# Kernel optimization log

Measured on AMD Instinct MI355X. Metric: run time of the kernel, lower is better.

Reference implementation:

```python
import jax, jax.numpy as jnp
import numpy as np

EMBEDDING_DIM = 128


def _position_encoding_init(n_position, emb_dim):
    # positions 1..n_position, angle[pos, j] = pos / 10000^(2*(j//2)/emb_dim)
    pos = jnp.arange(1, n_position + 1, dtype=jnp.float32)[:, None]  # [S,1]
    j = jnp.arange(emb_dim, dtype=jnp.float32)[None, :]              # [1,D]
    angle = pos / jnp.power(10000.0, 2.0 * jnp.floor(j / 2.0) / emb_dim)  # [S,D]
    # faithful to the original: rows 1: get sin/cos, row 0 stays raw
    pe = angle
    pe = pe.at[1:, 0::2].set(jnp.sin(angle[1:, 0::2]))
    pe = pe.at[1:, 1::2].set(jnp.cos(angle[1:, 1::2]))
    return pe.astype(jnp.float32)


def setup_inputs() -> dict:
    key = jax.random.key(0)
    k1, k2, k3 = jax.random.split(key, 3)
    B, S = 128, 2048
    x = jax.random.normal(k1, (B, S, 2), dtype=jnp.float32)
    # solutions / best_solutions must be permutations of 0..S-1 per row
    solutions = jax.vmap(lambda k: jax.random.permutation(k, S))(jax.random.split(k2, B)).astype(jnp.int64)
    best_solutions = jax.vmap(lambda k: jax.random.permutation(k, S))(jax.random.split(k3, B)).astype(jnp.int64)
    return {"x": x, "solutions": solutions, "best_solutions": best_solutions}


def reference(x, solutions, best_solutions):
    B, S = solutions.shape
    pe = _position_encoding_init(S, EMBEDDING_DIM)  # [S, D]
    # visited_time[b, i] = position at which node i is visited = argsort of the tour
    visited_time = jnp.argsort(solutions, axis=1)            # [B, S]
    best_visited_time = jnp.argsort(best_solutions, axis=1)  # [B, S]
    pos_enc = pe[visited_time]            # [B, S, D] gather over the table
    best_pos_enc = pe[best_visited_time]  # [B, S, D]
    return pos_enc, best_pos_enc
```

## Files before the change

kernel.cpp:

```cpp
#include <hip/hip_runtime.h>
#include <math.h>

#define BB 128
#define SS 2048
#define DD 128
#define BS (BB * SS)
#define BLOCKS 8192
#define ROWSTRIDE (BLOCKS * 8)

typedef float f4 __attribute__((ext_vector_type(4)));

__global__ __launch_bounds__(256) void fused_scatter_kernel(
        const int* __restrict__ sol, const int* __restrict__ best,
        float* __restrict__ out) {
    const int t    = threadIdx.x;
    const int lane = t & 31;
    const int rib  = t >> 5;
    const int base = blockIdx.x * 8 + rib;
    const int i    = base & (SS - 1);

    const float c = -13.287712379549449f / 64.0f;
    const float invf0 = exp2f(c * (float)(2 * lane));
    const float invf1 = exp2f(c * (float)(2 * lane + 1));
    const float a0 = (float)(i + 1) * invf0;
    const float a1 = (float)(i + 1) * invf1;
    f4 v;
    if (i == 0) {
        v[0] = a0; v[1] = a0; v[2] = a1; v[3] = a1;
    } else {
        float s0, c0, s1, c1;
        sincosf(a0, &s0, &c0);
        sincosf(a1, &s1, &c1);
        v[0] = s0; v[1] = c0; v[2] = s1; v[3] = c1;
    }

    #pragma unroll
    for (int h = 0; h < 2; ++h) {
        const int* __restrict__ perm = h ? best : sol;
        float* __restrict__ outh = out + (size_t)h * BS * DD;
        #pragma unroll
        for (int it = 0; it < 4; ++it) {
            const int k    = base + it * ROWSTRIDE;
            const int node = perm[k];
            const int dstRow = (k - i) + node;
            ((f4*)(outh + (size_t)dstRow * DD))[lane] = v;
        }
    }
}

extern "C" void kernel_launch(void* const* d_in, const int* in_sizes, int n_in,
                              void* d_out, int out_size, void* d_ws, size_t ws_size,
                              hipStream_t stream) {
    const int* sol  = (const int*)d_in[1];
    const int* best = (const int*)d_in[2];
    float* out = (float*)d_out;

    fused_scatter_kernel<<<BLOCKS, 256, 0, stream>>>(sol, best, out);

    (void)in_sizes; (void)n_in; (void)out_size; (void)d_ws; (void)ws_size;
}
```

Before: 45.96 us.

## Split into permutation inversion plus sequential-write gather with fast hardware trig

Inverts both permutations into a workspace buffer with a small scatter kernel, then runs a second kernel that writes output rows sequentially and computes the trig values per row using the hardware sin/cos builtins after range reduction. The goal is to replace scattered 512-byte row writes with coalesced sequential writes. It adds an extra launch and an int round-trip through memory. The hardware trig may also lose some accuracy for large angles. The old fused kernel is kept as a fallback when the workspace is too small.

Result: slower. 52.74 us (+14.7%).

```diff
diff --git a/kernel.cpp b/kernel.cpp
--- a/kernel.cpp
+++ b/kernel.cpp
@@ -5,10 +5,59 @@
 #define SS 2048
 #define DD 128
 #define BS (BB * SS)
-#define BLOCKS 8192
-#define ROWSTRIDE (BLOCKS * 8)
+#define GBLOCKS 8192
+#define RSTRIDE (GBLOCKS * 8)
 
 typedef float f4 __attribute__((ext_vector_type(4)));
+
+__global__ __launch_bounds__(256) void invert_kernel(
+        const int* __restrict__ sol, const int* __restrict__ best,
+        int* __restrict__ vt) {
+    const int idx = blockIdx.x * 256 + threadIdx.x;
+    const int half = (idx >= BS) ? 1 : 0;
+    const int k    = half ? idx - BS : idx;
+    const int i    = k & (SS - 1);
+    const int node = half ? best[k] : sol[k];
+    vt[half * BS + (k - i) + node] = i;
+}
+
+__global__ __launch_bounds__(256) void gather_trig_kernel(
+        const int* __restrict__ vt, float* __restrict__ out) {
+    const int t    = threadIdx.x;
+    const int lane = t & 31;
+    const int rib  = t >> 5;
+    const int base = blockIdx.x * 8 + rib;
+
+    const float c = -13.287712379549449f / 64.0f;
+    const float invf0 = exp2f(c * (float)(2 * lane));
+    const float invf1 = exp2f(c * (float)(2 * lane + 1));
+    const float INV2PI = 0.15915494309189535f;
+
+    int iv[8];
+    #pragma unroll
+    for (int it = 0; it < 8; ++it)
+        iv[it] = vt[base + it * RSTRIDE];
+
+    #pragma unroll
+    for (int it = 0; it < 8; ++it) {
+        const int i = iv[it];
+        const float a0 = (float)(i + 1) * invf0;
+        const float a1 = (float)(i + 1) * invf1;
+        f4 v;
+        if (i == 0) {
+            v[0] = a0; v[1] = a0; v[2] = a1; v[3] = a1;
+        } else {
+            float f0 = a0 * INV2PI; f0 -= floorf(f0);
+            float f1 = a1 * INV2PI; f1 -= floorf(f1);
+            v[0] = __builtin_amdgcn_sinf(f0);
+            v[1] = __builtin_amdgcn_cosf(f0);
+            v[2] = __builtin_amdgcn_sinf(f1);
+            v[3] = __builtin_amdgcn_cosf(f1);
+        }
+        const int r = base + it * RSTRIDE;
+        ((f4*)(out + (size_t)r * DD))[lane] = v;
+    }
+}
 
 __global__ __launch_bounds__(256) void fused_scatter_kernel(
         const int* __restrict__ sol, const int* __restrict__ best,
@@ -33,14 +82,13 @@
         sincosf(a1, &s1, &c1);
         v[0] = s0; v[1] = c0; v[2] = s1; v[3] = c1;
     }
-
     #pragma unroll
     for (int h = 0; h < 2; ++h) {
         const int* __restrict__ perm = h ? best : sol;
         float* __restrict__ outh = out + (size_t)h * BS * DD;
         #pragma unroll
         for (int it = 0; it < 4; ++it) {
-            const int k    = base + it * ROWSTRIDE;
+            const int k    = base + it * RSTRIDE;
             const int node = perm[k];
             const int dstRow = (k - i) + node;
             ((f4*)(outh + (size_t)dstRow * DD))[lane] = v;
@@ -55,7 +103,14 @@
     const int* best = (const int*)d_in[2];
     float* out = (float*)d_out;
 
-    fused_scatter_kernel<<<BLOCKS, 256, 0, stream>>>(sol, best, out);
+    const size_t vtBytes = (size_t)2 * BS * sizeof(int);
 
-    (void)in_sizes; (void)n_in; (void)out_size; (void)d_ws; (void)ws_size;
+    if (ws_size >= vtBytes) {
+        int* vt = (int*)d_ws;
+        invert_kernel<<<(2 * BS) / 256, 256, 0, stream>>>(sol, best, vt);
+        gather_trig_kernel<<<GBLOCKS, 256, 0, stream>>>(vt, out);
+    } else {
+        fused_scatter_kernel<<<GBLOCKS, 256, 0, stream>>>(sol, best, out);
+    }
+    (void)in_sizes; (void)n_in; (void)out_size;
 }
```
